# Kernel optimization log

Hardware: AMD Instinct MI355X
Metric: run time of the kernel (lower is better)

The kernel has to match this reference:

```python
import jax, jax.numpy as jnp
import numpy as np

SOBEL_X = jnp.array([[-1., 0., 1.], [-2., 0., 2.], [-1., 0., 1.]], dtype=jnp.float32)
SOBEL_Y = jnp.array([[-1., -2., -1.], [0., 0., 0.], [1., 2., 1.]], dtype=jnp.float32)


def _aggregate_similarity_cosine(t):
    # t: [B, 2, H, W] (normalized vector field)
    z = ((0, 0), (0, 0))
    up = jnp.pad(t[:, :, 1:, :], z + ((0, 1), (0, 0)))
    down = jnp.pad(t[:, :, :-1, :], z + ((1, 0), (0, 0)))
    left = jnp.pad(t[:, :, :, 1:], z + ((0, 0), (0, 1)))
    right = jnp.pad(t[:, :, :, :-1], z + ((0, 0), (1, 0)))
    nb = jnp.stack((up, down, left, right), axis=4)          # [B,2,H,W,4]
    dp = (t[..., None] * nb).sum(axis=1)                     # [B,H,W,4]
    return jnp.stack((dp.max(axis=-1), dp.min(axis=-1)), 1)  # [B,2,H,W]


def _grad_magnitude(x):
    # depthwise 3x3 Sobel conv, SAME padding, groups=C
    C = x.shape[1]
    kx = jnp.broadcast_to(SOBEL_X[None, None], (C, 1, 3, 3))
    ky = jnp.broadcast_to(SOBEL_Y[None, None], (C, 1, 3, 3))
    dn = ('NCHW', 'OIHW', 'NCHW')
    gx = jax.lax.conv_general_dilated(x, kx, (1, 1), ((1, 1), (1, 1)),
                                      dimension_numbers=dn, feature_group_count=C)
    gy = jax.lax.conv_general_dilated(x, ky, (1, 1), ((1, 1), (1, 1)),
                                      dimension_numbers=dn, feature_group_count=C)
    return jnp.sqrt(gx * gx + gy * gy)


def setup_inputs() -> dict:
    key = jax.random.key(0)
    x = jax.random.normal(key, (16, 3, 512, 512), dtype=jnp.float32)
    return {"x": x}


def reference(x):
    e = x[:, :2]                                      # [B,2,H,W]
    delta = x[:, 2:3]                                 # [B,1,H,W]
    magnitude = jnp.linalg.norm(e, axis=1, keepdims=True)
    angle = 0.5 * jnp.arctan2(e[:, 0], e[:, 1])[:, None]
    e_norm = e / magnitude
    cross_product = e[:, 0:1] * e[:, 1:2]
    similarity = _aggregate_similarity_cosine(e_norm)  # [B,2,H,W]
    out = jnp.concatenate([e, magnitude, angle, e_norm, cross_product, delta, similarity], axis=1)  # [B,10,H,W]
    out = jnp.concatenate([out, _grad_magnitude(out)], axis=1)  # [B,20,H,W]
    return out
```

## Files before the change

kernel.cpp:

```cpp
#include <hip/hip_runtime.h>
#include <hip/hip_fp16.h>
#include <math.h>

#define IMG_H 512
#define IMG_W 512
#define NIMG  16
#define HW    (IMG_H * IMG_W)

#define TH 16
#define TW 64
#define HTH (TH + 2)
#define HTW (TW + 2)
#define LPH 72
#define PAD 4
#define TILES_H (IMG_H / TH)
#define TILES_W (IMG_W / TW)

typedef float vfloat4 __attribute__((ext_vector_type(4)));

__device__ __forceinline__ float rcp_fast(float v) {
#if __has_builtin(__builtin_amdgcn_rcpf)
    return __builtin_amdgcn_rcpf(v);
#else
    return 1.0f / v;
#endif
}
__device__ __forceinline__ float rsq_fast(float v) {
#if __has_builtin(__builtin_amdgcn_rsqf)
    return __builtin_amdgcn_rsqf(v);
#else
    return rsqrtf(v);
#endif
}
__device__ __forceinline__ float sqrt_fast(float v) {
#if __has_builtin(__builtin_amdgcn_sqrtf)
    return __builtin_amdgcn_sqrtf(v);
#else
    return sqrtf(v);
#endif
}

__device__ __forceinline__ float fast_atan2f(float y, float x) {
    float ay = fabsf(y), ax = fabsf(x);
    float mx = fmaxf(ay, ax), mn = fminf(ay, ax);
    float a = mn * rcp_fast(mx);
    float s = a * a;
    float r = fmaf(fmaf(fmaf(0.0208351f, s, -0.085133f), s, 0.180141f), s, -0.3302995f);
    r = a * fmaf(r, s, 0.9998660f);
    if (ay > ax)  r = 1.57079632679f - r;
    if (x < 0.0f) r = 3.14159265359f - r;
    return copysignf(r, y);
}

__device__ __forceinline__ void load4h(const __half* p, float* dst) {
    float2 raw = *reinterpret_cast<const float2*>(p);
    __half2 a = *reinterpret_cast<__half2*>(&raw.x);
    __half2 b = *reinterpret_cast<__half2*>(&raw.y);
    float2 fa = __half22float2(a), fb = __half22float2(b);
    dst[0] = fa.x; dst[1] = fa.y; dst[2] = fb.x; dst[3] = fb.y;
}

__global__ __launch_bounds__(256, 6) void fused_kernel(const float* __restrict__ x,
                                                       float* __restrict__ out) {
    __shared__ __align__(16) __half lds[10][HTH * LPH];

    int bid0 = blockIdx.x;
    int bid  = (bid0 & 7) * (NIMG * TILES_H * TILES_W / 8) + (bid0 >> 3);

    int n   = bid / (TILES_H * TILES_W);
    int t   = bid - n * (TILES_H * TILES_W);
    int th  = t / TILES_W;
    int tw  = t - th * TILES_W;
    int h0  = th * TH;
    int w0  = tw * TW;

    const float* xb = x + (size_t)n * 3 * HW;
    int tid = threadIdx.x;

    for (int i = tid; i < HTH * HTW; i += 256) {
        int hr = i / HTW;
        int wc = i - hr * HTW;
        int h  = h0 + hr - 1;
        int w  = w0 + wc - 1;

        float e0 = 0.f, e1 = 0.f, m = 0.f, ang = 0.f, en0 = 0.f, en1 = 0.f;
        float cp = 0.f, dl = 0.f, smax = 0.f, smin = 0.f;

        if (h >= 0 && h < IMG_H && w >= 0 && w < IMG_W) {
            int rem = h * IMG_W + w;
            e0 = xb[rem];
            e1 = xb[HW + rem];
            dl = xb[2 * HW + rem];

            float s2 = fmaf(e0, e0, e1 * e1);
            m   = sqrt_fast(s2);
            float is = rsq_fast(s2);
            en0 = e0 * is;
            en1 = e1 * is;
            ang = 0.5f * fast_atan2f(e0, e1);
            cp  = e0 * e1;

            float dpu = 0.f, dpd = 0.f, dpl = 0.f, dpr = 0.f;
            if (h + 1 < IMG_H) {
                float a0 = xb[rem + IMG_W], a1 = xb[HW + rem + IMG_W];
                float mi = rsq_fast(fmaf(a0, a0, a1 * a1));
                dpu = fmaf(en0, a0 * mi, en1 * (a1 * mi));
            }
            if (h > 0) {
                float a0 = xb[rem - IMG_W], a1 = xb[HW + rem - IMG_W];
                float mi = rsq_fast(fmaf(a0, a0, a1 * a1));
                dpd = fmaf(en0, a0 * mi, en1 * (a1 * mi));
            }
            if (w + 1 < IMG_W) {
                float a0 = xb[rem + 1], a1 = xb[HW + rem + 1];
                float mi = rsq_fast(fmaf(a0, a0, a1 * a1));
                dpl = fmaf(en0, a0 * mi, en1 * (a1 * mi));
            }
            if (w > 0) {
                float a0 = xb[rem - 1], a1 = xb[HW + rem - 1];
                float mi = rsq_fast(fmaf(a0, a0, a1 * a1));
                dpr = fmaf(en0, a0 * mi, en1 * (a1 * mi));
            }
            smax = fmaxf(fmaxf(dpu, dpd), fmaxf(dpl, dpr));
            smin = fminf(fminf(dpu, dpd), fminf(dpl, dpr));
        }

        int li = hr * LPH + wc + PAD;
        lds[0][li] = __float2half(e0);
        lds[1][li] = __float2half(e1);
        lds[2][li] = __float2half(m);
        lds[3][li] = __float2half(ang);
        lds[4][li] = __float2half(en0);
        lds[5][li] = __float2half(en1);
        lds[6][li] = __float2half(cp);
        lds[7][li] = __float2half(dl);
        lds[8][li] = __float2half(smax);
        lds[9][li] = __float2half(smin);
    }

    __syncthreads();

    int r  = tid >> 4;
    int c  = tid & 15;
    int h  = h0 + r;
    int wa = w0 + 4 * c;
    float* op = out + (size_t)n * 20 * HW + (size_t)h * IMG_W + wa;

    int off = 4 * c + PAD;
    int rt = r * LPH + off;
    int rm = (r + 1) * LPH + off;
    int rb = (r + 2) * LPH + off;

#pragma unroll
    for (int ch = 0; ch < 10; ++ch) {
        const __half* L = lds[ch];

        float tt[8], mm[8], bb[8];
        load4h(&L[rt], tt); load4h(&L[rt + 4], tt + 4);
        load4h(&L[rm], mm); load4h(&L[rm + 4], mm + 4);
        load4h(&L[rb], bb); load4h(&L[rb + 4], bb + 4);

        float vs[6], dd[6];
#pragma unroll
        for (int j = 0; j < 6; ++j) {
            vs[j] = tt[j] + fmaf(2.0f, mm[j], bb[j]);
            dd[j] = bb[j] - tt[j];
        }

        vfloat4 mag;
        float gx, gy;
        gx = vs[2] - vs[0]; gy = fmaf(2.0f, dd[1], dd[0] + dd[2]);
        mag.x = sqrt_fast(fmaf(gx, gx, gy * gy));
        gx = vs[3] - vs[1]; gy = fmaf(2.0f, dd[2], dd[1] + dd[3]);
        mag.y = sqrt_fast(fmaf(gx, gx, gy * gy));
        gx = vs[4] - vs[2]; gy = fmaf(2.0f, dd[3], dd[2] + dd[4]);
        mag.z = sqrt_fast(fmaf(gx, gx, gy * gy));
        gx = vs[5] - vs[3]; gy = fmaf(2.0f, dd[4], dd[3] + dd[5]);
        mag.w = sqrt_fast(fmaf(gx, gx, gy * gy));

        vfloat4 cen;
        cen.x = mm[1]; cen.y = mm[2]; cen.z = mm[3]; cen.w = mm[4];

        __builtin_nontemporal_store(cen, reinterpret_cast<vfloat4*>(&op[(size_t)ch * HW]));
        __builtin_nontemporal_store(mag, reinterpret_cast<vfloat4*>(&op[(size_t)(10 + ch) * HW]));
    }
}

extern "C" void kernel_launch(void* const* d_in, const int* in_sizes, int n_in,
                              void* d_out, int out_size, void* d_ws, size_t ws_size,
                              hipStream_t stream) {
    const float* x = (const float*)d_in[0];
    float* out = (float*)d_out;

    int grid = NIMG * TILES_H * TILES_W;
    fused_kernel<<<grid, 256, 0, stream>>>(x, out);
}
```

Baseline: 74.72 us.

## Stage normalized vectors in shared memory with a wider halo for the similarity stencil

Adds a first pass that computes normalized e vectors once per pixel over a two-pixel halo and stores them as half2 in LDS. A second pass then computes the neighbor cosine max/min from LDS, replacing the four redundant global reloads and rsqrt calls per pixel. The e_norm channels are read from the packed half2 buffer for their Sobel output, and the remaining channels move into an 8-plane array. The cost is an extra barrier, a slightly larger halo region, and neighbor dot products that now use half-precision normalized values.

```diff
diff --git a/kernel.cpp b/kernel.cpp
--- a/kernel.cpp
+++ b/kernel.cpp
@@ -11,8 +11,12 @@
 #define TW 64
 #define HTH (TH + 2)
 #define HTW (TW + 2)
+#define ERH (TH + 4)
+#define ERW (TW + 4)
 #define LPH 72
 #define PAD 4
+#define EPS 72
+#define PADE 3
 #define TILES_H (IMG_H / TH)
 #define TILES_W (IMG_W / TW)
 
@@ -60,9 +64,46 @@
     dst[0] = fa.x; dst[1] = fa.y; dst[2] = fb.x; dst[3] = fb.y;
 }
 
+__device__ __forceinline__ void loadrow8(const __half2* p, float* a, float* b) {
+    union { vfloat4 v; __half2 h[4]; } u0, u1;
+    u0.v = *reinterpret_cast<const vfloat4*>(p);
+    u1.v = *reinterpret_cast<const vfloat4*>(p + 4);
+#pragma unroll
+    for (int j = 0; j < 4; ++j) {
+        float2 f = __half22float2(u0.h[j]);
+        a[j] = f.x; b[j] = f.y;
+    }
+#pragma unroll
+    for (int j = 0; j < 4; ++j) {
+        float2 f = __half22float2(u1.h[j]);
+        a[4 + j] = f.x; b[4 + j] = f.y;
+    }
+}
+
+__device__ __forceinline__ vfloat4 sobel4(const float* tt, const float* mm, const float* bb) {
+    float vs[6], dd[6];
+#pragma unroll
+    for (int j = 0; j < 6; ++j) {
+        vs[j] = tt[j] + fmaf(2.0f, mm[j], bb[j]);
+        dd[j] = bb[j] - tt[j];
+    }
+    vfloat4 mag;
+    float gx, gy;
+    gx = vs[2] - vs[0]; gy = fmaf(2.f, dd[1], dd[0] + dd[2]);
+    mag.x = sqrt_fast(fmaf(gx, gx, gy * gy));
+    gx = vs[3] - vs[1]; gy = fmaf(2.f, dd[2], dd[1] + dd[3]);
+    mag.y = sqrt_fast(fmaf(gx, gx, gy * gy));
+    gx = vs[4] - vs[2]; gy = fmaf(2.f, dd[3], dd[2] + dd[4]);
+    mag.z = sqrt_fast(fmaf(gx, gx, gy * gy));
+    gx = vs[5] - vs[3]; gy = fmaf(2.f, dd[4], dd[3] + dd[5]);
+    mag.w = sqrt_fast(fmaf(gx, gx, gy * gy));
+    return mag;
+}
+
 __global__ __launch_bounds__(256, 6) void fused_kernel(const float* __restrict__ x,
                                                        float* __restrict__ out) {
-    __shared__ __align__(16) __half lds[10][HTH * LPH];
+    __shared__ __align__(16) __half  lds[8][HTH * LPH];
+    __shared__ __align__(16) __half2 lden[ERH * EPS];
 
     int bid0 = blockIdx.x;
     int bid  = (bid0 & 7) * (NIMG * TILES_H * TILES_W / 8) + (bid0 >> 3);
@@ -77,67 +118,68 @@
     const float* xb = x + (size_t)n * 3 * HW;
     int tid = threadIdx.x;
 
+    for (int i = tid; i < ERH * ERW; i += 256) {
+        int er = i / ERW;
+        int ec = i - er * ERW;
+        int h  = h0 + er - 2;
+        int w  = w0 + ec - 2;
+        bool inimg = (h >= 0) && (h < IMG_H) && (w >= 0) && (w < IMG_W);
+        int rem = h * IMG_W + w;
+
+        float e0 = 0.f, e1 = 0.f, en0 = 0.f, en1 = 0.f;
+        if (inimg) {
+            e0 = xb[rem];
+            e1 = xb[HW + rem];
+            float is = rsq_fast(fmaf(e0, e0, e1 * e1));
+            en0 = e0 * is;
+            en1 = e1 * is;
+        }
+        lden[er * EPS + ec + PADE] = __floats2half2_rn(en0, en1);
+
+        int hr = er - 1, wc = ec - 1;
+        if (hr >= 0 && hr < HTH && wc >= 0 && wc < HTW) {
+            float dl = 0.f, m = 0.f, ang = 0.f, cp = 0.f;
+            if (inimg) {
+                dl = xb[2 * HW + rem];
+                float s2 = fmaf(e0, e0, e1 * e1);
+                m   = sqrt_fast(s2);
+                ang = 0.5f * fast_atan2f(e0, e1);
+                cp  = e0 * e1;
+            }
+            int li = hr * LPH + wc + PAD;
+            lds[0][li] = __float2half(e0);
+            lds[1][li] = __float2half(e1);
+            lds[2][li] = __float2half(m);
+            lds[3][li] = __float2half(ang);
+            lds[4][li] = __float2half(cp);
+            lds[5][li] = __float2half(dl);
+        }
+    }
+    __syncthreads();
+
     for (int i = tid; i < HTH * HTW; i += 256) {
         int hr = i / HTW;
         int wc = i - hr * HTW;
-        int h  = h0 + hr - 1;
-        int w  = w0 + wc - 1;
-
-        float e0 = 0.f, e1 = 0.f, m = 0.f, ang = 0.f, en0 = 0.f, en1 = 0.f;
-        float cp = 0.f, dl = 0.f, smax = 0.f, smin = 0.f;
-
-        if (h >= 0 && h < IMG_H && w >= 0 && w < IMG_W) {
-            int rem = h * IMG_W + w;
-            e0 = xb[rem];
-            e1 = xb[HW + rem];
-            dl = xb[2 * HW + rem];
-
-            float s2 = fmaf(e0, e0, e1 * e1);
-            m   = sqrt_fast(s2);
-            float is = rsq_fast(s2);
-            en0 = e0 * is;
-            en1 = e1 * is;
-            ang = 0.5f * fast_atan2f(e0, e1);
-            cp  = e0 * e1;
-
-            float dpu = 0.f, dpd = 0.f, dpl = 0.f, dpr = 0.f;
-            if (h + 1 < IMG_H) {
-                float a0 = xb[rem + IMG_W], a1 = xb[HW + rem + IMG_W];
-                float mi = rsq_fast(fmaf(a0, a0, a1 * a1));
-                dpu = fmaf(en0, a0 * mi, en1 * (a1 * mi));
-            }
-            if (h > 0) {
-                float a0 = xb[rem - IMG_W], a1 = xb[HW + rem - IMG_W];
-                float mi = rsq_fast(fmaf(a0, a0, a1 * a1));
-                dpd = fmaf(en0, a0 * mi, en1 * (a1 * mi));
-            }
-            if (w + 1 < IMG_W) {
-                float a0 = xb[rem + 1], a1 = xb[HW + rem + 1];
-                float mi = rsq_fast(fmaf(a0, a0, a1 * a1));
-                dpl = fmaf(en0, a0 * mi, en1 * (a1 * mi));
-            }
-            if (w > 0) {
-                float a0 = xb[rem - 1], a1 = xb[HW + rem - 1];
-                float mi = rsq_fast(fmaf(a0, a0, a1 * a1));
-                dpr = fmaf(en0, a0 * mi, en1 * (a1 * mi));
-            }
-            smax = fmaxf(fmaxf(dpu, dpd), fmaxf(dpl, dpr));
-            smin = fminf(fminf(dpu, dpd), fminf(dpl, dpr));
-        }
+        int eb = (hr + 1) * EPS + (wc + 1) + PADE;
+
+        float2 o  = __half22float2(lden[eb]);
+        float2 u  = __half22float2(lden[eb + EPS]);
+        float2 d  = __half22float2(lden[eb - EPS]);
+        float2 lf = __half22float2(lden[eb + 1]);
+        float2 rg = __half22float2(lden[eb - 1]);
+
+        float dpu = fmaf(o.x, u.x,  o.y * u.y);
+        float dpd = fmaf(o.x, d.x,  o.y * d.y);
+        float dpl = fmaf(o.x, lf.x, o.y * lf.y);
+        float dpr = fmaf(o.x, rg.x, o.y * rg.y);
+
+        float smax = fmaxf(fmaxf(dpu, dpd), fmaxf(dpl, dpr));
+        float smin = fminf(fminf(dpu, dpd), fminf(dpl, dpr));
 
         int li = hr * LPH + wc + PAD;
-        lds[0][li] = __float2half(e0);
-        lds[1][li] = __float2half(e1);
-        lds[2][li] = __float2half(m);
-        lds[3][li] = __float2half(ang);
-        lds[4][li] = __float2half(en0);
-        lds[5][li] = __float2half(en1);
-        lds[6][li] = __float2half(cp);
-        lds[7][li] = __float2half(dl);
-        lds[8][li] = __float2half(smax);
-        lds[9][li] = __float2half(smin);
-    }
-
+        lds[6][li] = __float2half(smax);
+        lds[7][li] = __float2half(smin);
+    }
     __syncthreads();
 
     int r  = tid >> 4;
@@ -151,38 +193,42 @@
     int rm = (r + 1) * LPH + off;
     int rb = (r + 2) * LPH + off;
 
-#pragma unroll
-    for (int ch = 0; ch < 10; ++ch) {
-        const __half* L = lds[ch];
-
+    const int outch[8] = {0, 1, 2, 3, 6, 7, 8, 9};
+
+#pragma unroll
+    for (int p = 0; p < 8; ++p) {
+        const __half* L = lds[p];
         float tt[8], mm[8], bb[8];
         load4h(&L[rt], tt); load4h(&L[rt + 4], tt + 4);
         load4h(&L[rm], mm); load4h(&L[rm + 4], mm + 4);
         load4h(&L[rb], bb); load4h(&L[rb + 4], bb + 4);
 
-        float vs[6], dd[6];
-#pragma unroll
-        for (int j = 0; j < 6; ++j) {
-            vs[j] = tt[j] + fmaf(2.0f, mm[j], bb[j]);
-            dd[j] = bb[j] - tt[j];
-        }
-
-        vfloat4 mag;
-        float gx, gy;
-        gx = vs[2] - vs[0]; gy = fmaf(2.0f, dd[1], dd[0] + dd[2]);
-        mag.x = sqrt_fast(fmaf(gx, gx, gy * gy));
-        gx = vs[3] - vs[1]; gy = fmaf(2.0f, dd[2], dd[1] + dd[3]);
-        mag.y = sqrt_fast(fmaf(gx, gx, gy * gy));
-        gx = vs[4] - vs[2]; gy = fmaf(2.0f, dd[3], dd[2] + dd[4]);
-        mag.z = sqrt_fast(fmaf(gx, gx, gy * gy));
-        gx = vs[5] - vs[3]; gy = fmaf(2.0f, dd[4], dd[3] + dd[5]);
-        mag.w = sqrt_fast(fmaf(gx, gx, gy * gy));
-
+        vfloat4 mag = sobel4(tt, mm, bb);
         vfloat4 cen;
         cen.x = mm[1]; cen.y = mm[2]; cen.z = mm[3]; cen.w = mm[4];
 
+        int ch = outch[p];
         __builtin_nontemporal_store(cen, reinterpret_cast<vfloat4*>(&op[(size_t)ch * HW]));
         __builtin_nontemporal_store(mag, reinterpret_cast<vfloat4*>(&op[(size_t)(10 + ch) * HW]));
+    }
+
+    {
+        int eb0 = (r + 1) * EPS + 4 * c + 4;
+        float ta[8], tb[8], ma[8], mb[8], ba[8], bb2[8];
+        loadrow8(&lden[eb0],            ta, tb);
+        loadrow8(&lden[eb0 + EPS],      ma, mb);
+        loadrow8(&lden[eb0 + 2 * EPS],  ba, bb2);
+
+        vfloat4 mag4 = sobel4(ta, ma, ba);
+        vfloat4 mag5 = sobel4(tb, mb, bb2);
+        vfloat4 cen4, cen5;
+        cen4.x = ma[1]; cen4.y = ma[2]; cen4.z = ma[3]; cen4.w = ma[4];
+        cen5.x = mb[1]; cen5.y = mb[2]; cen5.z = mb[3]; cen5.w = mb[4];
+
+        __builtin_nontemporal_store(cen4, reinterpret_cast<vfloat4*>(&op[(size_t)4 * HW]));
+        __builtin_nontemporal_store(mag4, reinterpret_cast<vfloat4*>(&op[(size_t)14 * HW]));
+        __builtin_nontemporal_store(cen5, reinterpret_cast<vfloat4*>(&op[(size_t)5 * HW]));
+        __builtin_nontemporal_store(mag5, reinterpret_cast<vfloat4*>(&op[(size_t)15 * HW]));
     }
 }
 
```

Result: faster. 70.41 us (-5.8%).
